# Kernel optimization log

Hardware: AMD Instinct MI355X
Metric: run time of the kernel (lower is better)

The kernel has to match this reference:

```python
import jax, jax.numpy as jnp
import numpy as np

N_NODES = 100000
N_EDGES = 1600000
IN_CH = 128
HID = 64


def gcn_conv(x, W, b, src, dst, n):
    """PyG-style GCNConv: add self-loops, symmetric deg^-1/2 normalization."""
    h = x @ W  # [n, out]
    # degree including self-loop, computed from destination (col) indices
    deg = jax.ops.segment_sum(jnp.ones_like(dst, dtype=h.dtype), dst, num_segments=n) + 1.0
    dinv = jax.lax.rsqrt(deg)  # [n]
    norm = dinv[src] * dinv[dst]  # [E]
    agg = jax.ops.segment_sum(h[src] * norm[:, None], dst, num_segments=n)
    agg = agg + h * (1.0 / deg)[:, None]  # self-loop term: norm = 1/deg
    return agg + b


def setup_inputs() -> dict:
    key = jax.random.key(0)
    ks = jax.random.split(key, 6)
    x = jax.random.normal(ks[0], (N_NODES, IN_CH), dtype=jnp.float32)
    edge_index = jax.random.randint(ks[1], (2, N_EDGES), 0, N_NODES, dtype=jnp.int64)
    W1 = jax.random.normal(ks[2], (IN_CH, HID), dtype=jnp.float32) / np.sqrt(IN_CH)
    b1 = jnp.zeros((HID,), dtype=jnp.float32)
    W2 = jax.random.normal(ks[3], (HID, HID), dtype=jnp.float32) / np.sqrt(HID)
    b2 = jnp.zeros((HID,), dtype=jnp.float32)
    Wl = jax.random.normal(ks[4], (HID, 1), dtype=jnp.float32) / np.sqrt(HID)
    bl = jnp.zeros((1,), dtype=jnp.float32)
    return {"x": x, "edge_index": edge_index, "W1": W1, "b1": b1,
            "W2": W2, "b2": b2, "Wl": Wl, "bl": bl}


def reference(x, edge_index, W1, b1, W2, b2, Wl, bl):
    src, dst = edge_index[0], edge_index[1]
    n = x.shape[0]
    h = gcn_conv(x, W1, b1, src, dst, n)
    h = jax.nn.relu(h)
    # dropout: identity in eval mode
    h = gcn_conv(h, W2, b2, src, dst, n)
    h = jax.nn.relu(h)
    out = (h @ Wl + bl)[:, 0]  # [n]
    return out
```

## Files before the change

kernel.cpp:

```cpp
#include <hip/hip_runtime.h>
#include <hip/hip_fp16.h>


#define SHIFT 9
#define BSZ   (1 << SHIFT)
#define NBMAX 256
#define BIN_CH 2048
#define BCAP  12288
#define OCAP  1024

using f16x8 = __attribute__((ext_vector_type(8))) _Float16;
using f16x2 = __attribute__((ext_vector_type(2))) _Float16;
using f32x4 = __attribute__((ext_vector_type(4))) float;

__global__ __launch_bounds__(256) void k_bin(const int* __restrict__ src,
                                             const int* __restrict__ dst,
                                             int* __restrict__ bcursor,
                                             unsigned* __restrict__ binned,
                                             __half* __restrict__ hs, int n, int E) {
    if (blockIdx.x == 0 && threadIdx.x < 8) {
        uint4 z = {0u, 0u, 0u, 0u};
        reinterpret_cast<uint4*>(hs + ((size_t)n << 6))[threadIdx.x] = z;
    }
    __shared__ int h[NBMAX];
    __shared__ int base[NBMAX];
    const int beg = blockIdx.x * BIN_CH;
    const int end = min(beg + BIN_CH, E);
    for (int i = threadIdx.x; i < NBMAX; i += 256) h[i] = 0;
    __syncthreads();
    for (int e = beg + threadIdx.x; e < end; e += 256)
        atomicAdd(&h[dst[e] >> SHIFT], 1);
    __syncthreads();
    for (int i = threadIdx.x; i < NBMAX; i += 256) {
        base[i] = h[i] ? atomicAdd(&bcursor[i], h[i]) : 0;
        h[i] = 0;
    }
    __syncthreads();
    for (int e = beg + threadIdx.x; e < end; e += 256) {
        int d = dst[e];
        int b = d >> SHIFT;
        int off = atomicAdd(&h[b], 1);
        binned[(size_t)b * BCAP + base[b] + off] =
            (unsigned)src[e] | ((unsigned)(d & (BSZ - 1)) << 17);
    }
}

__global__ __launch_bounds__(256) void k_bfill(const unsigned* __restrict__ binned,
                                               const int* __restrict__ counts,
                                               int* __restrict__ rowptr,
                                               int* __restrict__ cfix,
                                               int* __restrict__ ovf,
                                               float* __restrict__ dinv, int n) {
    __shared__ int cnt[BSZ];
    __shared__ int cur[BSZ];
    __shared__ int obase[BSZ];
    __shared__ int stmp[256];
    const int b = blockIdx.x;
    const int t = threadIdx.x;
    const int ecnt = counts[b];
    const unsigned* bp = binned + (size_t)b * BCAP;
    for (int i = t; i < BSZ; i += 256) { cnt[i] = 0; cur[i] = 0; }
    __syncthreads();
    for (int e = t; e < ecnt; e += 256)
        atomicAdd(&cnt[bp[e] >> 17], 1);
    __syncthreads();
    int v0 = max(cnt[2 * t] - 32, 0), v1 = max(cnt[2 * t + 1] - 32, 0);
    int s = v0 + v1;
    stmp[t] = s;
    __syncthreads();
    for (int off = 1; off < 256; off <<= 1) {
        int u = (t >= off) ? stmp[t - off] : 0;
        __syncthreads();
        stmp[t] += u;
        __syncthreads();
    }
    int ex = stmp[t] - s;
    obase[2 * t] = ex;
    obase[2 * t + 1] = ex + v0;
    __syncthreads();
    const int gbase = b << SHIFT;
    const int dum = (int)((unsigned)n << 7);
    for (int j = t; j < BSZ; j += 256) {
        int g = gbase + j;
        if (g < n) {
            int dg = cnt[j];
            rowptr[g] = (int)(((unsigned)(b * OCAP + obase[j]) << 8) |
                              (unsigned)min(dg, 255));
            dinv[g] = rsqrtf((float)dg + 1.0f);
        }
    }
    for (int sx = t; sx < BSZ * 32; sx += 256) {
        int j = sx >> 5, slot = sx & 31;
        int g = gbase + j;
        if (g < n && slot >= cnt[j]) cfix[(size_t)g * 32 + slot] = dum;
    }
    for (int e = t; e < ecnt; e += 256) {
        unsigned pv = bp[e];
        int j = pv >> 17;
        int off = atomicAdd(&cur[j], 1);
        int so = (int)((pv & 0x1FFFFu) << 7);
        if (off < 32) cfix[(size_t)(gbase + j) * 32 + off] = so;
        else          ovf[b * OCAP + obase[j] + off - 32] = so;
    }
}

template <int K, bool A_FP32>
__global__ __launch_bounds__(256) void k_gemm_mfma(const void* __restrict__ Av,
                                                   const float* __restrict__ W,
                                                   const float* __restrict__ dinv,
                                                   __half* __restrict__ C, int n) {
    constexpr int KP = K + 8;
    __shared__ _Float16 Wt[64 * KP];
    const int tid = threadIdx.x;
    for (int i = tid; i < K * 64; i += 256) {
        int k = i >> 6, c = i & 63;
        Wt[c * KP + k] = (_Float16)W[i];
    }
    __syncthreads();

    const int lane = tid & 63;
    const int wv = tid >> 6;
    const int r16 = lane & 15;
    const int kq = lane >> 4;
    const int rb = blockIdx.x * 64 + wv * 16;
    const int arow = min(rb + r16, n - 1);

    f32x4 acc[4] = {{0.f,0.f,0.f,0.f},{0.f,0.f,0.f,0.f},
                    {0.f,0.f,0.f,0.f},{0.f,0.f,0.f,0.f}};

#pragma unroll
    for (int kk = 0; kk < K; kk += 32) {
        f16x8 a;
        if (A_FP32) {
            const float* Ap = (const float*)Av + (size_t)arow * K + kk + kq * 8;
            float4 f0 = *reinterpret_cast<const float4*>(Ap);
            float4 f1 = *reinterpret_cast<const float4*>(Ap + 4);
            a[0] = (_Float16)f0.x; a[1] = (_Float16)f0.y;
            a[2] = (_Float16)f0.z; a[3] = (_Float16)f0.w;
            a[4] = (_Float16)f1.x; a[5] = (_Float16)f1.y;
            a[6] = (_Float16)f1.z; a[7] = (_Float16)f1.w;
        } else {
            const _Float16* Ap = (const _Float16*)Av + (size_t)arow * K + kk + kq * 8;
            a = *reinterpret_cast<const f16x8*>(Ap);
        }
#pragma unroll
        for (int nt = 0; nt < 4; ++nt) {
            f16x8 b = *reinterpret_cast<const f16x8*>(&Wt[(nt * 16 + r16) * KP + kk + kq * 8]);
            acc[nt] = __builtin_amdgcn_mfma_f32_16x16x32_f16(a, b, acc[nt], 0, 0, 0);
        }
    }

#pragma unroll
    for (int r = 0; r < 4; ++r) {
        const int row = rb + kq * 4 + r;
        if (row < n) {
            const float di = dinv[row];
#pragma unroll
            for (int nt = 0; nt < 4; ++nt)
                C[((size_t)row << 6) + nt * 16 + r16] = __float2half(acc[nt][r] * di);
        }
    }
}

__device__ __forceinline__ void dotu4(float acc[8], uint4 u, f16x2 pl, f16x2 ph) {
    union { uint4 u4; f16x2 h[4]; } v;
    v.u4 = u;
    acc[0] = __builtin_amdgcn_fdot2(v.h[0], pl, acc[0], false);
    acc[1] = __builtin_amdgcn_fdot2(v.h[0], ph, acc[1], false);
    acc[2] = __builtin_amdgcn_fdot2(v.h[1], pl, acc[2], false);
    acc[3] = __builtin_amdgcn_fdot2(v.h[1], ph, acc[3], false);
    acc[4] = __builtin_amdgcn_fdot2(v.h[2], pl, acc[4], false);
    acc[5] = __builtin_amdgcn_fdot2(v.h[2], ph, acc[5], false);
    acc[6] = __builtin_amdgcn_fdot2(v.h[3], pl, acc[6], false);
    acc[7] = __builtin_amdgcn_fdot2(v.h[3], ph, acc[7], false);
}

__device__ __forceinline__ void fold8(float acc[8]) {
#pragma unroll
    for (int m = 8; m <= 32; m <<= 1) {
#pragma unroll
        for (int j = 0; j < 8; ++j)
            acc[j] += __shfl_xor(acc[j], m, 64);
    }
}

__device__ __forceinline__ void tail_node(const char* __restrict__ hsb,
                                          const int* __restrict__ ovf,
                                          unsigned pk, int g, int p,
                                          unsigned dum, float acc[8],
                                          f16x2 pl, f16x2 ph) {
    const int deg = (int)(pk & 255u);
    if (deg <= 32) return;
    const int obeg = (int)(pk >> 8);
    const int t = deg - g;
    const unsigned poff = (unsigned)(p << 4);
    const unsigned dumo = dum + poff;
    const int ns = (deg + 7) >> 3;
    for (int k = 4; k < ns; k += 4) {
        const int ik = obeg + 8 * (k - 4) + g;
        unsigned c0 = (unsigned)ovf[ik]      + poff;
        unsigned c1 = (unsigned)ovf[ik + 8]  + poff;
        unsigned c2 = (unsigned)ovf[ik + 16] + poff;
        unsigned c3 = (unsigned)ovf[ik + 24] + poff;
        const int kb = 8 * k;
        uint4 u0 = *reinterpret_cast<const uint4*>(hsb + ((kb      < t) ? c0 : dumo));
        uint4 u1 = *reinterpret_cast<const uint4*>(hsb + ((kb + 8  < t) ? c1 : dumo));
        uint4 u2 = *reinterpret_cast<const uint4*>(hsb + ((kb + 16 < t) ? c2 : dumo));
        uint4 u3 = *reinterpret_cast<const uint4*>(hsb + ((kb + 24 < t) ? c3 : dumo));
        dotu4(acc, u0, pl, ph);
        dotu4(acc, u1, pl, ph);
        dotu4(acc, u2, pl, ph);
        dotu4(acc, u3, pl, ph);
    }
}

__device__ __forceinline__ void gather_quad(const char* __restrict__ hsb,
                                            const int* __restrict__ cfix,
                                            const int* __restrict__ ovf,
                                            int ic0, int ic1, int ic2, int ic3,
                                            unsigned pk0, unsigned pk1,
                                            unsigned pk2, unsigned pk3,
                                            int g, int p, unsigned dum,
                                            float a0[8], float a1[8],
                                            float a2[8], float a3[8]) {
    const f16x2 pl = {(_Float16)1.0f, (_Float16)0.0f};
    const f16x2 ph = {(_Float16)0.0f, (_Float16)1.0f};
    const unsigned poff = (unsigned)(p << 4);
    const int b0 = ic0 * 32 + g;
    const int b1 = ic1 * 32 + g;
    const int b2 = ic2 * 32 + g;
    const int b3 = ic3 * 32 + g;
    unsigned oa0 = (unsigned)cfix[b0]      + poff;
    unsigned oa1 = (unsigned)cfix[b0 + 8]  + poff;
    unsigned oa2 = (unsigned)cfix[b0 + 16] + poff;
    unsigned oa3 = (unsigned)cfix[b0 + 24] + poff;
    unsigned ob0 = (unsigned)cfix[b1]      + poff;
    unsigned ob1 = (unsigned)cfix[b1 + 8]  + poff;
    unsigned ob2 = (unsigned)cfix[b1 + 16] + poff;
    unsigned ob3 = (unsigned)cfix[b1 + 24] + poff;
    unsigned oc0 = (unsigned)cfix[b2]      + poff;
    unsigned oc1 = (unsigned)cfix[b2 + 8]  + poff;
    unsigned oc2 = (unsigned)cfix[b2 + 16] + poff;
    unsigned oc3 = (unsigned)cfix[b2 + 24] + poff;
    unsigned od0 = (unsigned)cfix[b3]      + poff;
    unsigned od1 = (unsigned)cfix[b3 + 8]  + poff;
    unsigned od2 = (unsigned)cfix[b3 + 16] + poff;
    unsigned od3 = (unsigned)cfix[b3 + 24] + poff;
    uint4 ua0 = *reinterpret_cast<const uint4*>(hsb + oa0);
    uint4 ua1 = *reinterpret_cast<const uint4*>(hsb + oa1);
    uint4 ua2 = *reinterpret_cast<const uint4*>(hsb + oa2);
    uint4 ua3 = *reinterpret_cast<const uint4*>(hsb + oa3);
    uint4 ub0 = *reinterpret_cast<const uint4*>(hsb + ob0);
    uint4 ub1 = *reinterpret_cast<const uint4*>(hsb + ob1);
    uint4 ub2 = *reinterpret_cast<const uint4*>(hsb + ob2);
    uint4 ub3 = *reinterpret_cast<const uint4*>(hsb + ob3);
    uint4 uc0 = *reinterpret_cast<const uint4*>(hsb + oc0);
    uint4 uc1 = *reinterpret_cast<const uint4*>(hsb + oc1);
    uint4 uc2 = *reinterpret_cast<const uint4*>(hsb + oc2);
    uint4 uc3 = *reinterpret_cast<const uint4*>(hsb + oc3);
    uint4 ud0 = *reinterpret_cast<const uint4*>(hsb + od0);
    uint4 ud1 = *reinterpret_cast<const uint4*>(hsb + od1);
    uint4 ud2 = *reinterpret_cast<const uint4*>(hsb + od2);
    uint4 ud3 = *reinterpret_cast<const uint4*>(hsb + od3);
    dotu4(a0, ua0, pl, ph);
    dotu4(a0, ua1, pl, ph);
    dotu4(a0, ua2, pl, ph);
    dotu4(a0, ua3, pl, ph);
    dotu4(a1, ub0, pl, ph);
    dotu4(a1, ub1, pl, ph);
    dotu4(a1, ub2, pl, ph);
    dotu4(a1, ub3, pl, ph);
    dotu4(a2, uc0, pl, ph);
    dotu4(a2, uc1, pl, ph);
    dotu4(a2, uc2, pl, ph);
    dotu4(a2, uc3, pl, ph);
    dotu4(a3, ud0, pl, ph);
    dotu4(a3, ud1, pl, ph);
    dotu4(a3, ud2, pl, ph);
    dotu4(a3, ud3, pl, ph);
    tail_node(hsb, ovf, pk0, g, p, dum, a0, pl, ph);
    tail_node(hsb, ovf, pk1, g, p, dum, a1, pl, ph);
    tail_node(hsb, ovf, pk2, g, p, dum, a2, pl, ph);
    tail_node(hsb, ovf, pk3, g, p, dum, a3, pl, ph);
    fold8(a0);
    fold8(a1);
    fold8(a2);
    fold8(a3);
}

__device__ __forceinline__ void sel4(float a[8], int nsel, const float a0[8],
                                     const float a1[8], const float a2[8],
                                     const float a3[8]) {
#pragma unroll
    for (int j = 0; j < 8; ++j) {
        float x01 = (nsel & 1) ? a1[j] : a0[j];
        float x23 = (nsel & 1) ? a3[j] : a2[j];
        a[j] = (nsel & 2) ? x23 : x01;
    }
}

__global__ __launch_bounds__(256) void k_agg_relu(const __half* __restrict__ hs,
                                                  const int* __restrict__ rowptr,
                                                  const int* __restrict__ cfix,
                                                  const int* __restrict__ ovf,
                                                  const float* __restrict__ dinv,
                                                  const float* __restrict__ b,
                                                  __half* __restrict__ out, int n) {
    const int wv = threadIdx.x >> 6;
    const int i0 = blockIdx.x * 16 + wv * 4;
    const int lane = threadIdx.x & 63;
    if (i0 >= n) return;
    const int g = lane >> 3, p = lane & 7;
    const int ic0 = i0;
    const int ic1 = min(i0 + 1, n - 1);
    const int ic2 = min(i0 + 2, n - 1);
    const int ic3 = min(i0 + 3, n - 1);
    const int nsel = g & 3;
    const int it = i0 + nsel;
    const int iw = min(it, n - 1);
    const unsigned pk0 = (unsigned)rowptr[ic0];
    const unsigned pk1 = (unsigned)rowptr[ic1];
    const unsigned pk2 = (unsigned)rowptr[ic2];
    const unsigned pk3 = (unsigned)rowptr[ic3];
    uint4 su = *reinterpret_cast<const uint4*>(hs + ((size_t)iw << 6) + (p << 3));
    const float di = dinv[iw];
    float a0[8] = {}, a1[8] = {}, a2[8] = {}, a3[8] = {};
    gather_quad((const char*)hs, cfix, ovf, ic0, ic1, ic2, ic3,
                pk0, pk1, pk2, pk3, g, p, (unsigned)n << 7, a0, a1, a2, a3);
    if (lane < 32 && it < n) {
        const f16x2 pl = {(_Float16)1.0f, (_Float16)0.0f};
        const f16x2 ph = {(_Float16)0.0f, (_Float16)1.0f};
        float a[8];
        sel4(a, nsel, a0, a1, a2, a3);
        dotu4(a, su, pl, ph);
        float4 b0 = *reinterpret_cast<const float4*>(b + (p << 3));
        float4 b1 = *reinterpret_cast<const float4*>(b + (p << 3) + 4);
        __half2 h0 = __halves2half2(__float2half(fmaxf(fmaf(a[0], di, b0.x), 0.f)),
                                    __float2half(fmaxf(fmaf(a[1], di, b0.y), 0.f)));
        __half2 h1 = __halves2half2(__float2half(fmaxf(fmaf(a[2], di, b0.z), 0.f)),
                                    __float2half(fmaxf(fmaf(a[3], di, b0.w), 0.f)));
        __half2 h2 = __halves2half2(__float2half(fmaxf(fmaf(a[4], di, b1.x), 0.f)),
                                    __float2half(fmaxf(fmaf(a[5], di, b1.y), 0.f)));
        __half2 h3 = __halves2half2(__float2half(fmaxf(fmaf(a[6], di, b1.z), 0.f)),
                                    __float2half(fmaxf(fmaf(a[7], di, b1.w), 0.f)));
        uint4 u;
        u.x = *reinterpret_cast<unsigned*>(&h0);
        u.y = *reinterpret_cast<unsigned*>(&h1);
        u.z = *reinterpret_cast<unsigned*>(&h2);
        u.w = *reinterpret_cast<unsigned*>(&h3);
        *reinterpret_cast<uint4*>(out + ((size_t)it << 6) + (p << 3)) = u;
    }
}

__global__ __launch_bounds__(256) void k_agg_head(const __half* __restrict__ hs,
                                                  const int* __restrict__ rowptr,
                                                  const int* __restrict__ cfix,
                                                  const int* __restrict__ ovf,
                                                  const float* __restrict__ dinv,
                                                  const float* __restrict__ b2,
                                                  const float* __restrict__ Wl,
                                                  const float* __restrict__ bl,
                                                  float* __restrict__ out, int n) {
    const int wv = threadIdx.x >> 6;
    const int i0 = blockIdx.x * 16 + wv * 4;
    const int lane = threadIdx.x & 63;
    if (i0 >= n) return;
    const int g = lane >> 3, p = lane & 7;
    const int ic0 = i0;
    const int ic1 = min(i0 + 1, n - 1);
    const int ic2 = min(i0 + 2, n - 1);
    const int ic3 = min(i0 + 3, n - 1);
    const int nsel = g & 3;
    const int it = i0 + nsel;
    const int iw = min(it, n - 1);
    const unsigned pk0 = (unsigned)rowptr[ic0];
    const unsigned pk1 = (unsigned)rowptr[ic1];
    const unsigned pk2 = (unsigned)rowptr[ic2];
    const unsigned pk3 = (unsigned)rowptr[ic3];
    uint4 su = *reinterpret_cast<const uint4*>(hs + ((size_t)iw << 6) + (p << 3));
    const float di = dinv[iw];
    float a0[8] = {}, a1[8] = {}, a2[8] = {}, a3[8] = {};
    gather_quad((const char*)hs, cfix, ovf, ic0, ic1, ic2, ic3,
                pk0, pk1, pk2, pk3, g, p, (unsigned)n << 7, a0, a1, a2, a3);
    const f16x2 pl = {(_Float16)1.0f, (_Float16)0.0f};
    const f16x2 ph = {(_Float16)0.0f, (_Float16)1.0f};
    float a[8];
    sel4(a, nsel, a0, a1, a2, a3);
    dotu4(a, su, pl, ph);
    float4 b0 = *reinterpret_cast<const float4*>(b2 + (p << 3));
    float4 b1 = *reinterpret_cast<const float4*>(b2 + (p << 3) + 4);
    float4 w0 = *reinterpret_cast<const float4*>(Wl + (p << 3));
    float4 w1 = *reinterpret_cast<const float4*>(Wl + (p << 3) + 4);
    float v = fmaxf(fmaf(a[0], di, b0.x), 0.f) * w0.x
            + fmaxf(fmaf(a[1], di, b0.y), 0.f) * w0.y
            + fmaxf(fmaf(a[2], di, b0.z), 0.f) * w0.z
            + fmaxf(fmaf(a[3], di, b0.w), 0.f) * w0.w
            + fmaxf(fmaf(a[4], di, b1.x), 0.f) * w1.x
            + fmaxf(fmaf(a[5], di, b1.y), 0.f) * w1.y
            + fmaxf(fmaf(a[6], di, b1.z), 0.f) * w1.z
            + fmaxf(fmaf(a[7], di, b1.w), 0.f) * w1.w;
    v += __shfl_xor(v, 1, 64);
    v += __shfl_xor(v, 2, 64);
    v += __shfl_xor(v, 4, 64);
    if (p == 0 && g < 4 && it < n) out[it] = v + bl[0];
}

extern "C" void kernel_launch(void* const* d_in, const int* in_sizes, int n_in,
                              void* d_out, int out_size, void* d_ws, size_t ws_size,
                              hipStream_t stream) {
    const float* x  = (const float*)d_in[0];
    const int*   ei = (const int*)d_in[1];
    const float* W1 = (const float*)d_in[2];
    const float* b1 = (const float*)d_in[3];
    const float* W2 = (const float*)d_in[4];
    const float* b2 = (const float*)d_in[5];
    const float* Wl = (const float*)d_in[6];
    const float* bl = (const float*)d_in[7];
    float* out = (float*)d_out;

    const int n = in_sizes[0] / 128;
    const int E = in_sizes[1] / 2;
    const int* src = ei;
    const int* dst = ei + E;
    const int nb = (n + BSZ - 1) >> SHIFT;

    char* ws = (char*)d_ws;
    size_t o = 0;
    auto alloc = [&](size_t bytes) {
        void* p = ws + o;
        o = (o + bytes + 255) & ~(size_t)255;
        return p;
    };
    float* dinv    = (float*)alloc((size_t)n * 4);
    int*   bcursor = (int*)  alloc((size_t)NBMAX * 4);
    int*   rowptr  = (int*)  alloc((size_t)(n + 1) * 4);
    int*   cfix    = (int*)  alloc((size_t)n * 32 * 4);
    int*   ovf     = (int*)  alloc(((size_t)nb * OCAP + 64) * 4);
    __half* hs     = (__half*)alloc((size_t)(n + 1) * 64 * 2);
    __half* bufA   = (__half*)alloc((size_t)n * 64 * 2);
    unsigned* binned = (unsigned*)alloc((size_t)nb * BCAP * 4);

    hipMemsetAsync(bcursor, 0, NBMAX * sizeof(int), stream);
    k_bin<<<(E + BIN_CH - 1) / BIN_CH, 256, 0, stream>>>(src, dst, bcursor, binned,
                                                         hs, n, E);
    k_bfill<<<nb, 256, 0, stream>>>(binned, bcursor, rowptr, cfix, ovf, dinv, n);

    k_gemm_mfma<128, true><<<(n + 63) / 64, 256, 0, stream>>>(x, W1, dinv, hs, n);
    k_agg_relu<<<(n + 15) / 16, 256, 0, stream>>>(hs, rowptr, cfix, ovf, dinv, b1,
                                                  bufA, n);

    k_gemm_mfma<64, false><<<(n + 63) / 64, 256, 0, stream>>>(bufA, W2, dinv, hs, n);
    k_agg_head<<<(n + 15) / 16, 256, 0, stream>>>(hs, rowptr, cfix, ovf, dinv, b2,
                                                  Wl, bl, out, n);
}
```

Before: 156.9 us.

## Replace two-pass binned CSR build with direct atomic slot scatter and global overflow list

Drops the bin-then-fill graph preprocessing (two kernels with a shared-memory histogram, scan and staging buffer) in favour of a single kernel that does a global atomicAdd per edge on a per-node counter and writes the source straight into a fixed 32-slot row. Edges beyond 32 go to a small global overflow list that the aggregation kernels scan linearly when any of the four nodes has degree over 32. The zero row moves to index 0, so zeroed slots double as the padding sentinel, and the whole count and slot table is cleared with one memset. This trades a staging round-trip for random global atomics and a memset of the full slot table, and the overflow scan and OVCAP cap add risk with skewed degrees.

```diff
diff --git a/kernel.cpp b/kernel.cpp
--- a/kernel.cpp
+++ b/kernel.cpp
@@ -2,106 +2,55 @@
 #include <hip/hip_fp16.h>
 
 
-#define SHIFT 9
-#define BSZ   (1 << SHIFT)
-#define NBMAX 256
-#define BIN_CH 2048
-#define BCAP  12288
-#define OCAP  1024
+#define SLOTS 32
+#define OVCAP 8192
 
 using f16x8 = __attribute__((ext_vector_type(8))) _Float16;
 using f16x2 = __attribute__((ext_vector_type(2))) _Float16;
 using f32x4 = __attribute__((ext_vector_type(4))) float;
 
-__global__ __launch_bounds__(256) void k_bin(const int* __restrict__ src,
-                                             const int* __restrict__ dst,
-                                             int* __restrict__ bcursor,
-                                             unsigned* __restrict__ binned,
-                                             __half* __restrict__ hs, int n, int E) {
+__global__ __launch_bounds__(256) void k_scatter(const int* __restrict__ src,
+                                                 const int* __restrict__ dst,
+                                                 int* __restrict__ cnt,
+                                                 int* __restrict__ cfix,
+                                                 int* __restrict__ ovlist,
+                                                 int* __restrict__ ovn,
+                                                 __half* __restrict__ hs, int E) {
     if (blockIdx.x == 0 && threadIdx.x < 8) {
         uint4 z = {0u, 0u, 0u, 0u};
-        reinterpret_cast<uint4*>(hs + ((size_t)n << 6))[threadIdx.x] = z;
-    }
-    __shared__ int h[NBMAX];
-    __shared__ int base[NBMAX];
-    const int beg = blockIdx.x * BIN_CH;
-    const int end = min(beg + BIN_CH, E);
-    for (int i = threadIdx.x; i < NBMAX; i += 256) h[i] = 0;
-    __syncthreads();
-    for (int e = beg + threadIdx.x; e < end; e += 256)
-        atomicAdd(&h[dst[e] >> SHIFT], 1);
-    __syncthreads();
-    for (int i = threadIdx.x; i < NBMAX; i += 256) {
-        base[i] = h[i] ? atomicAdd(&bcursor[i], h[i]) : 0;
-        h[i] = 0;
-    }
-    __syncthreads();
-    for (int e = beg + threadIdx.x; e < end; e += 256) {
-        int d = dst[e];
-        int b = d >> SHIFT;
-        int off = atomicAdd(&h[b], 1);
-        binned[(size_t)b * BCAP + base[b] + off] =
-            (unsigned)src[e] | ((unsigned)(d & (BSZ - 1)) << 17);
-    }
-}
-
-__global__ __launch_bounds__(256) void k_bfill(const unsigned* __restrict__ binned,
-                                               const int* __restrict__ counts,
-                                               int* __restrict__ rowptr,
-                                               int* __restrict__ cfix,
-                                               int* __restrict__ ovf,
-                                               float* __restrict__ dinv, int n) {
-    __shared__ int cnt[BSZ];
-    __shared__ int cur[BSZ];
-    __shared__ int obase[BSZ];
-    __shared__ int stmp[256];
-    const int b = blockIdx.x;
-    const int t = threadIdx.x;
-    const int ecnt = counts[b];
-    const unsigned* bp = binned + (size_t)b * BCAP;
-    for (int i = t; i < BSZ; i += 256) { cnt[i] = 0; cur[i] = 0; }
-    __syncthreads();
-    for (int e = t; e < ecnt; e += 256)
-        atomicAdd(&cnt[bp[e] >> 17], 1);
-    __syncthreads();
-    int v0 = max(cnt[2 * t] - 32, 0), v1 = max(cnt[2 * t + 1] - 32, 0);
-    int s = v0 + v1;
-    stmp[t] = s;
-    __syncthreads();
-    for (int off = 1; off < 256; off <<= 1) {
-        int u = (t >= off) ? stmp[t - off] : 0;
-        __syncthreads();
-        stmp[t] += u;
-        __syncthreads();
-    }
-    int ex = stmp[t] - s;
-    obase[2 * t] = ex;
-    obase[2 * t + 1] = ex + v0;
-    __syncthreads();
-    const int gbase = b << SHIFT;
-    const int dum = (int)((unsigned)n << 7);
-    for (int j = t; j < BSZ; j += 256) {
-        int g = gbase + j;
-        if (g < n) {
-            int dg = cnt[j];
-            rowptr[g] = (int)(((unsigned)(b * OCAP + obase[j]) << 8) |
-                              (unsigned)min(dg, 255));
-            dinv[g] = rsqrtf((float)dg + 1.0f);
-        }
-    }
-    for (int sx = t; sx < BSZ * 32; sx += 256) {
-        int j = sx >> 5, slot = sx & 31;
-        int g = gbase + j;
-        if (g < n && slot >= cnt[j]) cfix[(size_t)g * 32 + slot] = dum;
-    }
-    for (int e = t; e < ecnt; e += 256) {
-        unsigned pv = bp[e];
-        int j = pv >> 17;
-        int off = atomicAdd(&cur[j], 1);
-        int so = (int)((pv & 0x1FFFFu) << 7);
-        if (off < 32) cfix[(size_t)(gbase + j) * 32 + off] = so;
-        else          ovf[b * OCAP + obase[j] + off - 32] = so;
-    }
+        reinterpret_cast<uint4*>(hs)[threadIdx.x] = z;
+    }
+    const int e4 = (blockIdx.x * 256 + threadIdx.x) * 4;
+    if (e4 >= E) return;
+    const int4 d4 = *reinterpret_cast<const int4*>(dst + e4);
+    const int4 s4 = *reinterpret_cast<const int4*>(src + e4);
+    int o0 = atomicAdd(&cnt[d4.x], 1);
+    int o1 = atomicAdd(&cnt[d4.y], 1);
+    int o2 = atomicAdd(&cnt[d4.z], 1);
+    int o3 = atomicAdd(&cnt[d4.w], 1);
+    int v0 = (s4.x + 1) << 7;
+    int v1 = (s4.y + 1) << 7;
+    int v2 = (s4.z + 1) << 7;
+    int v3 = (s4.w + 1) << 7;
+    if (o0 < SLOTS) cfix[d4.x * SLOTS + o0] = v0;
+    else { int oi = atomicAdd(ovn, 1); if (oi < OVCAP) { ovlist[2*oi] = d4.x; ovlist[2*oi+1] = v0; } }
+    if (o1 < SLOTS) cfix[d4.y * SLOTS + o1] = v1;
+    else { int oi = atomicAdd(ovn, 1); if (oi < OVCAP) { ovlist[2*oi] = d4.y; ovlist[2*oi+1] = v1; } }
+    if (o2 < SLOTS) cfix[d4.z * SLOTS + o2] = v2;
+    else { int oi = atomicAdd(ovn, 1); if (oi < OVCAP) { ovlist[2*oi] = d4.z; ovlist[2*oi+1] = v2; } }
+    if (o3 < SLOTS) cfix[d4.w * SLOTS + o3] = v3;
+    else { int oi = atomicAdd(ovn, 1); if (oi < OVCAP) { ovlist[2*oi] = d4.w; ovlist[2*oi+1] = v3; } }
+}
+
+__global__ __launch_bounds__(256) void k_post(const int* __restrict__ cnt,
+                                              float* __restrict__ dinv,
+                                              unsigned char* __restrict__ degc,
+                                              int n) {
+    const int i = blockIdx.x * 256 + threadIdx.x;
+    if (i >= n) return;
+    const int dg = cnt[i];
+    dinv[i] = rsqrtf((float)dg + 1.0f);
+    degc[i] = (unsigned char)min(dg, 255);
 }
 
 template <int K, bool A_FP32>
@@ -184,52 +133,19 @@
     }
 }
 
-__device__ __forceinline__ void tail_node(const char* __restrict__ hsb,
-                                          const int* __restrict__ ovf,
-                                          unsigned pk, int g, int p,
-                                          unsigned dum, float acc[8],
-                                          f16x2 pl, f16x2 ph) {
-    const int deg = (int)(pk & 255u);
-    if (deg <= 32) return;
-    const int obeg = (int)(pk >> 8);
-    const int t = deg - g;
-    const unsigned poff = (unsigned)(p << 4);
-    const unsigned dumo = dum + poff;
-    const int ns = (deg + 7) >> 3;
-    for (int k = 4; k < ns; k += 4) {
-        const int ik = obeg + 8 * (k - 4) + g;
-        unsigned c0 = (unsigned)ovf[ik]      + poff;
-        unsigned c1 = (unsigned)ovf[ik + 8]  + poff;
-        unsigned c2 = (unsigned)ovf[ik + 16] + poff;
-        unsigned c3 = (unsigned)ovf[ik + 24] + poff;
-        const int kb = 8 * k;
-        uint4 u0 = *reinterpret_cast<const uint4*>(hsb + ((kb      < t) ? c0 : dumo));
-        uint4 u1 = *reinterpret_cast<const uint4*>(hsb + ((kb + 8  < t) ? c1 : dumo));
-        uint4 u2 = *reinterpret_cast<const uint4*>(hsb + ((kb + 16 < t) ? c2 : dumo));
-        uint4 u3 = *reinterpret_cast<const uint4*>(hsb + ((kb + 24 < t) ? c3 : dumo));
-        dotu4(acc, u0, pl, ph);
-        dotu4(acc, u1, pl, ph);
-        dotu4(acc, u2, pl, ph);
-        dotu4(acc, u3, pl, ph);
-    }
-}
-
 __device__ __forceinline__ void gather_quad(const char* __restrict__ hsb,
                                             const int* __restrict__ cfix,
-                                            const int* __restrict__ ovf,
                                             int ic0, int ic1, int ic2, int ic3,
-                                            unsigned pk0, unsigned pk1,
-                                            unsigned pk2, unsigned pk3,
-                                            int g, int p, unsigned dum,
+                                            int g, int p,
                                             float a0[8], float a1[8],
                                             float a2[8], float a3[8]) {
     const f16x2 pl = {(_Float16)1.0f, (_Float16)0.0f};
     const f16x2 ph = {(_Float16)0.0f, (_Float16)1.0f};
     const unsigned poff = (unsigned)(p << 4);
-    const int b0 = ic0 * 32 + g;
-    const int b1 = ic1 * 32 + g;
-    const int b2 = ic2 * 32 + g;
-    const int b3 = ic3 * 32 + g;
+    const int b0 = ic0 * SLOTS + g;
+    const int b1 = ic1 * SLOTS + g;
+    const int b2 = ic2 * SLOTS + g;
+    const int b3 = ic3 * SLOTS + g;
     unsigned oa0 = (unsigned)cfix[b0]      + poff;
     unsigned oa1 = (unsigned)cfix[b0 + 8]  + poff;
     unsigned oa2 = (unsigned)cfix[b0 + 16] + poff;
@@ -278,14 +194,28 @@
     dotu4(a3, ud1, pl, ph);
     dotu4(a3, ud2, pl, ph);
     dotu4(a3, ud3, pl, ph);
-    tail_node(hsb, ovf, pk0, g, p, dum, a0, pl, ph);
-    tail_node(hsb, ovf, pk1, g, p, dum, a1, pl, ph);
-    tail_node(hsb, ovf, pk2, g, p, dum, a2, pl, ph);
-    tail_node(hsb, ovf, pk3, g, p, dum, a3, pl, ph);
-    fold8(a0);
-    fold8(a1);
-    fold8(a2);
-    fold8(a3);
+}
+
+__device__ __forceinline__ void tail_scan(const char* __restrict__ hsb,
+                                          const int* __restrict__ ovlist, int K,
+                                          int ic0, int ic1, int ic2, int ic3,
+                                          int g, int p,
+                                          float a0[8], float a1[8],
+                                          float a2[8], float a3[8]) {
+    if (g != 0) return;
+    const f16x2 pl = {(_Float16)1.0f, (_Float16)0.0f};
+    const f16x2 ph = {(_Float16)0.0f, (_Float16)1.0f};
+    const unsigned poff = (unsigned)(p << 4);
+    for (int j = 0; j < K; ++j) {
+        int d = ovlist[2 * j];
+        if (d != ic0 && d != ic1 && d != ic2 && d != ic3) continue;
+        unsigned v = (unsigned)ovlist[2 * j + 1] + poff;
+        uint4 u = *reinterpret_cast<const uint4*>(hsb + v);
+        if (d == ic0) dotu4(a0, u, pl, ph);
+        else if (d == ic1) dotu4(a1, u, pl, ph);
+        else if (d == ic2) dotu4(a2, u, pl, ph);
+        else dotu4(a3, u, pl, ph);
+    }
 }
 
 __device__ __forceinline__ void sel4(float a[8], int nsel, const float a0[8],
@@ -300,9 +230,10 @@
 }
 
 __global__ __launch_bounds__(256) void k_agg_relu(const __half* __restrict__ hs,
-                                                  const int* __restrict__ rowptr,
                                                   const int* __restrict__ cfix,
-                                                  const int* __restrict__ ovf,
+                                                  const unsigned char* __restrict__ degc,
+                                                  const int* __restrict__ ovlist,
+                                                  const int* __restrict__ ovn,
                                                   const float* __restrict__ dinv,
                                                   const float* __restrict__ b,
                                                   __half* __restrict__ out, int n) {
@@ -318,15 +249,21 @@
     const int nsel = g & 3;
     const int it = i0 + nsel;
     const int iw = min(it, n - 1);
-    const unsigned pk0 = (unsigned)rowptr[ic0];
-    const unsigned pk1 = (unsigned)rowptr[ic1];
-    const unsigned pk2 = (unsigned)rowptr[ic2];
-    const unsigned pk3 = (unsigned)rowptr[ic3];
-    uint4 su = *reinterpret_cast<const uint4*>(hs + ((size_t)iw << 6) + (p << 3));
+    uint4 su = *reinterpret_cast<const uint4*>(hs + (((size_t)iw + 1) << 6) + (p << 3));
     const float di = dinv[iw];
     float a0[8] = {}, a1[8] = {}, a2[8] = {}, a3[8] = {};
-    gather_quad((const char*)hs, cfix, ovf, ic0, ic1, ic2, ic3,
-                pk0, pk1, pk2, pk3, g, p, (unsigned)n << 7, a0, a1, a2, a3);
+    gather_quad((const char*)hs, cfix, ic0, ic1, ic2, ic3, g, p, a0, a1, a2, a3);
+    const int dmax = max(max((int)degc[ic0], (int)degc[ic1]),
+                         max((int)degc[ic2], (int)degc[ic3]));
+    if (dmax > SLOTS) {
+        int K = min(ovn[0], OVCAP);
+        tail_scan((const char*)hs, ovlist, K, ic0, ic1, ic2, ic3, g, p,
+                  a0, a1, a2, a3);
+    }
+    fold8(a0);
+    fold8(a1);
+    fold8(a2);
+    fold8(a3);
     if (lane < 32 && it < n) {
         const f16x2 pl = {(_Float16)1.0f, (_Float16)0.0f};
         const f16x2 ph = {(_Float16)0.0f, (_Float16)1.0f};
@@ -353,9 +290,10 @@
 }
 
 __global__ __launch_bounds__(256) void k_agg_head(const __half* __restrict__ hs,
-                                                  const int* __restrict__ rowptr,
                                                   const int* __restrict__ cfix,
-                                                  const int* __restrict__ ovf,
+                                                  const unsigned char* __restrict__ degc,
+                                                  const int* __restrict__ ovlist,
+                                                  const int* __restrict__ ovn,
                                                   const float* __restrict__ dinv,
                                                   const float* __restrict__ b2,
                                                   const float* __restrict__ Wl,
@@ -373,15 +311,21 @@
     const int nsel = g & 3;
     const int it = i0 + nsel;
     const int iw = min(it, n - 1);
-    const unsigned pk0 = (unsigned)rowptr[ic0];
-    const unsigned pk1 = (unsigned)rowptr[ic1];
-    const unsigned pk2 = (unsigned)rowptr[ic2];
-    const unsigned pk3 = (unsigned)rowptr[ic3];
-    uint4 su = *reinterpret_cast<const uint4*>(hs + ((size_t)iw << 6) + (p << 3));
+    uint4 su = *reinterpret_cast<const uint4*>(hs + (((size_t)iw + 1) << 6) + (p << 3));
     const float di = dinv[iw];
     float a0[8] = {}, a1[8] = {}, a2[8] = {}, a3[8] = {};
-    gather_quad((const char*)hs, cfix, ovf, ic0, ic1, ic2, ic3,
-                pk0, pk1, pk2, pk3, g, p, (unsigned)n << 7, a0, a1, a2, a3);
+    gather_quad((const char*)hs, cfix, ic0, ic1, ic2, ic3, g, p, a0, a1, a2, a3);
+    const int dmax = max(max((int)degc[ic0], (int)degc[ic1]),
+                         max((int)degc[ic2], (int)degc[ic3]));
+    if (dmax > SLOTS) {
+        int K = min(ovn[0], OVCAP);
+        tail_scan((const char*)hs, ovlist, K, ic0, ic1, ic2, ic3, g, p,
+                  a0, a1, a2, a3);
+    }
+    fold8(a0);
+    fold8(a1);
+    fold8(a2);
+    fold8(a3);
     const f16x2 pl = {(_Float16)1.0f, (_Float16)0.0f};
     const f16x2 ph = {(_Float16)0.0f, (_Float16)1.0f};
     float a[8];
@@ -422,7 +366,6 @@
     const int E = in_sizes[1] / 2;
     const int* src = ei;
     const int* dst = ei + E;
-    const int nb = (n + BSZ - 1) >> SHIFT;
 
     char* ws = (char*)d_ws;
     size_t o = 0;
@@ -431,25 +374,26 @@
         o = (o + bytes + 255) & ~(size_t)255;
         return p;
     };
-    float* dinv    = (float*)alloc((size_t)n * 4);
-    int*   bcursor = (int*)  alloc((size_t)NBMAX * 4);
-    int*   rowptr  = (int*)  alloc((size_t)(n + 1) * 4);
-    int*   cfix    = (int*)  alloc((size_t)n * 32 * 4);
-    int*   ovf     = (int*)  alloc(((size_t)nb * OCAP + 64) * 4);
-    __half* hs     = (__half*)alloc((size_t)(n + 1) * 64 * 2);
-    __half* bufA   = (__half*)alloc((size_t)n * 64 * 2);
-    unsigned* binned = (unsigned*)alloc((size_t)nb * BCAP * 4);
-
-    hipMemsetAsync(bcursor, 0, NBMAX * sizeof(int), stream);
-    k_bin<<<(E + BIN_CH - 1) / BIN_CH, 256, 0, stream>>>(src, dst, bcursor, binned,
-                                                         hs, n, E);
-    k_bfill<<<nb, 256, 0, stream>>>(binned, bcursor, rowptr, cfix, ovf, dinv, n);
-
-    k_gemm_mfma<128, true><<<(n + 63) / 64, 256, 0, stream>>>(x, W1, dinv, hs, n);
-    k_agg_relu<<<(n + 15) / 16, 256, 0, stream>>>(hs, rowptr, cfix, ovf, dinv, b1,
-                                                  bufA, n);
-
-    k_gemm_mfma<64, false><<<(n + 63) / 64, 256, 0, stream>>>(bufA, W2, dinv, hs, n);
-    k_agg_head<<<(n + 15) / 16, 256, 0, stream>>>(hs, rowptr, cfix, ovf, dinv, b2,
-                                                  Wl, bl, out, n);
-}
+    int*   cnt  = (int*)alloc((size_t)n * 4);
+    int*   ovn  = (int*)alloc(256);
+    int*   cfix = (int*)alloc((size_t)n * SLOTS * 4);
+    size_t zbytes = (size_t)((char*)cfix + (size_t)n * SLOTS * 4 - (char*)cnt);
+    int*   ovlist = (int*)alloc((size_t)OVCAP * 2 * 4);
+    float* dinv   = (float*)alloc((size_t)n * 4);
+    unsigned char* degc = (unsigned char*)alloc((size_t)n);
+    __half* hs    = (__half*)alloc((size_t)(n + 1) * 64 * 2);
+    __half* bufA  = (__half*)alloc((size_t)n * 64 * 2);
+
+    hipMemsetAsync(cnt, 0, zbytes, stream);
+    k_scatter<<<(E / 4 + 255) / 256, 256, 0, stream>>>(src, dst, cnt, cfix,
+                                                       ovlist, ovn, hs, E);
+    k_post<<<(n + 255) / 256, 256, 0, stream>>>(cnt, dinv, degc, n);
+
+    k_gemm_mfma<128, true><<<(n + 63) / 64, 256, 0, stream>>>(x, W1, dinv, hs + 64, n);
+    k_agg_relu<<<(n + 15) / 16, 256, 0, stream>>>(hs, cfix, degc, ovlist, ovn,
+                                                  dinv, b1, bufA, n);
+
+    k_gemm_mfma<64, false><<<(n + 63) / 64, 256, 0, stream>>>(bufA, W2, dinv, hs + 64, n);
+    k_agg_head<<<(n + 15) / 16, 256, 0, stream>>>(hs, cfix, degc, ovlist, ovn,
+                                                  dinv, b2, Wl, bl, out, n);
+}
```

Result: slower. 233.8 us (+49.0%).
